# Kernel optimization log

Hardware: AMD Instinct MI355X
Metric: run time of the kernel (lower is better)

## Reference

```python
import jax, jax.numpy as jnp
import numpy as np

N, P, T, K = 20000, 5, 16, 3
IN, H, O = 150, 64, 128


def setup_inputs() -> dict:
    key = jax.random.key(0)
    k1, k2, k3, k4, k5 = jax.random.split(key, 5)
    x = jax.random.normal(k1, (N, IN), dtype=jnp.float32)
    conn_idx = jax.random.randint(k2, (N, P, T, K), 0, N, dtype=jnp.int32)
    conn_w = jax.random.uniform(k3, (N, P, T, K), dtype=jnp.float32)
    # learned params
    W1 = jax.random.normal(k4, (H, IN), dtype=jnp.float32) * 0.05   # linear_1 (no bias)
    Wg = jax.random.normal(k5, (O, H, P, T), dtype=jnp.float32) * 0.05  # geodesic conv weight
    bg = jnp.zeros((O,), dtype=jnp.float32)                          # geodesic conv bias
    return {"x": x, "conn_idx": conn_idx, "conn_w": conn_w, "W1": W1, "Wg": Wg, "bg": bg}


def reference(x, conn_idx, conn_w, W1, Wg, bg):
    # Linear + ReLU: [N, H]
    h = jax.nn.relu(x @ W1.T)
    # Geodesic patch gather: interpolate vertex features into P x T bins
    g = jnp.take(h, conn_idx, axis=0)                 # [N, P, T, K, H]
    patches = jnp.einsum('nptk,nptkh->npth', conn_w, g)  # [N, P, T, H]
    # Geodesic convolution: contract patch bins and channels
    out = jnp.einsum('npth,ohpt->no', patches, Wg) + bg  # [N, O]
    # L2 normalize per vertex
    norm = jnp.linalg.norm(out, axis=-1, keepdims=True)
    return out / norm
```

## Files before the change

### kernel.cpp

```cpp
#include <hip/hip_runtime.h>
#include <hip/hip_fp16.h>

#define NV   20000
#define KK   3
#define INF  150
#define HH   64
#define OO   128
#define PT   80
#define KTOT 5120
#define NB   64
#define RS   72
#define CB   (NB * RS)
#define XS   168
#define NBIN 20

typedef _Float16 fh8 __attribute__((ext_vector_type(8)));
typedef __attribute__((ext_vector_type(4))) float f32x4;
typedef __attribute__((ext_vector_type(8))) unsigned short u16x8;

__device__ __forceinline__ unsigned short f2h(float f) {
    return __half_as_ushort(__float2half(f));
}
__device__ __forceinline__ float h2f(unsigned short u) {
    return __half2float(__ushort_as_half(u));
}
__device__ __forceinline__ _Float16 u2h(unsigned short u) {
    union { unsigned short s; _Float16 h; } c; c.s = u; return c.h;
}

__global__ __launch_bounds__(256) void prep_kernel(
    const float* __restrict__ Wg, const float* __restrict__ x,
    const float* __restrict__ W1, unsigned short* __restrict__ W2,
    unsigned short* __restrict__ hb) {
    __shared__ __align__(16) unsigned char smem[32256];
    const int tid = threadIdx.x;

    if (blockIdx.x < 128) {
        float* lds = (float*)smem;
        const int o = blockIdx.x;
        const float* src = Wg + o * KTOT;
        for (int t = tid; t < KTOT; t += 256) {
            int h = t / 80, bin = t - h * 80;
            lds[h * 81 + bin] = src[t];
        }
        __syncthreads();
        for (int t = tid; t < KTOT; t += 256) {
            W2[(t >> 5) * 4096 + o * 32 + (t & 31)] =
                f2h(lds[(t & 63) * 81 + (t >> 6)]);
        }
        return;
    }

    unsigned short* xs = (unsigned short*)smem;
    unsigned short* ws = xs + 32 * XS;
    const int n0 = (blockIdx.x - 128) * 32;

    for (int e = tid; e < 32 * INF; e += 256) {
        int r = e / INF, c = e - r * INF;
        xs[r * XS + c] = f2h(x[n0 * INF + e]);
    }
    for (int e = tid; e < 32 * 18; e += 256) {
        int r = e / 18, c = e - r * 18;
        xs[r * XS + 150 + c] = 0;
    }
    for (int e = tid; e < 64 * INF; e += 256) {
        int r = e / INF, c = e - r * INF;
        ws[r * XS + c] = f2h(W1[e]);
    }
    for (int e = tid; e < 64 * 18; e += 256) {
        int r = e / 18, c = e - r * 18;
        ws[r * XS + 150 + c] = 0;
    }
    __syncthreads();

    const int wv   = tid >> 6;
    const int lane = tid & 63;
    const int q    = lane >> 4;
    const int r16  = lane & 15;
    const int o0   = wv * 16;

    f32x4 acc0 = {0.f, 0.f, 0.f, 0.f};
    f32x4 acc1 = acc0;
    #pragma unroll
    for (int s = 0; s < 5; s++) {
        const int kb = s * 32 + q * 8;
        fh8 a0 = *(const fh8*)(xs + r16 * XS + kb);
        fh8 a1 = *(const fh8*)(xs + (16 + r16) * XS + kb);
        fh8 b  = *(const fh8*)(ws + (o0 + r16) * XS + kb);
        acc0 = __builtin_amdgcn_mfma_f32_16x16x32_f16(a0, b, acc0, 0, 0, 0);
        acc1 = __builtin_amdgcn_mfma_f32_16x16x32_f16(a1, b, acc1, 0, 0, 0);
    }
    #pragma unroll
    for (int r = 0; r < 4; r++) {
        float v0 = acc0[r] > 0.f ? acc0[r] : 0.f;
        float v1 = acc1[r] > 0.f ? acc1[r] : 0.f;
        hb[(n0 + q * 4 + r) * HH + o0 + r16]      = f2h(v0);
        hb[(n0 + 16 + q * 4 + r) * HH + o0 + r16] = f2h(v1);
    }
}

__global__ __launch_bounds__(256, 4) void geo_kernel(
    const int*   __restrict__ conn_idx, const float* __restrict__ conn_w,
    const unsigned short* __restrict__ W2, const unsigned short* __restrict__ hb,
    float* __restrict__ out, unsigned short* __restrict__ parts) {
    __shared__ __align__(16) unsigned short pch[2 * CB];
    __shared__ __align__(16) unsigned short cp[NB * NBIN * 8];

    const int tid  = threadIdx.x;
    const int ks   = blockIdx.x & 3;
    const int n0   = (blockIdx.x >> 2) * NB;
    const int wv   = tid >> 6;
    const int lane = tid & 63;
    const int q    = lane >> 4;
    const int r16  = lane & 15;
    const int j8   = tid & 7;
    const int v0   = tid >> 3;
    const int bbase = ks * NBIN;
    const int Sbase = ks * 40;

    for (int e = tid; e < NB * NBIN; e += 256) {
        const int v = e / NBIN, cc = e - v * NBIN;
        const int vv = n0 + v;
        u16x8 pk = {0, 0, 0, 0, 0, 0, 0, 0};
        if (vv < NV) {
            const int g = vv * (PT * KK) + (bbase + cc) * KK;
            pk[0] = (unsigned short)conn_idx[g];
            pk[1] = (unsigned short)conn_idx[g + 1];
            pk[2] = (unsigned short)conn_idx[g + 2];
            pk[3] = f2h(conn_w[g]);
            pk[4] = f2h(conn_w[g + 1]);
            pk[5] = f2h(conn_w[g + 2]);
        }
        *(u16x8*)(cp + e * 8) = pk;
    }

    f32x4 acc[4][2];
    #pragma unroll
    for (int m = 0; m < 4; m++) {
        acc[m][0] = (f32x4){0.f, 0.f, 0.f, 0.f};
        acc[m][1] = (f32x4){0.f, 0.f, 0.f, 0.f};
    }

    u16x8 pa, pb;
    fh8   hva0, hva1, hva2, hvb0, hvb1, hvb2;

    auto loadg = [&](int cc) {
        pa = *(const u16x8*)(cp + (v0 * NBIN + cc) * 8);
        pb = *(const u16x8*)(cp + ((v0 + 32) * NBIN + cc) * 8);
        hva0 = *(const fh8*)(hb + (int)pa[0] * HH + j8 * 8);
        hva1 = *(const fh8*)(hb + (int)pa[1] * HH + j8 * 8);
        hva2 = *(const fh8*)(hb + (int)pa[2] * HH + j8 * 8);
        hvb0 = *(const fh8*)(hb + (int)pb[0] * HH + j8 * 8);
        hvb1 = *(const fh8*)(hb + (int)pb[1] * HH + j8 * 8);
        hvb2 = *(const fh8*)(hb + (int)pb[2] * HH + j8 * 8);
    };
    auto cwr = [&](unsigned short* buf) {
        const _Float16 a0 = u2h(pa[3]), a1 = u2h(pa[4]), a2 = u2h(pa[5]);
        const _Float16 b0 = u2h(pb[3]), b1 = u2h(pb[4]), b2 = u2h(pb[5]);
        const fh8 A0 = {a0, a0, a0, a0, a0, a0, a0, a0};
        const fh8 A1 = {a1, a1, a1, a1, a1, a1, a1, a1};
        const fh8 A2 = {a2, a2, a2, a2, a2, a2, a2, a2};
        const fh8 B0 = {b0, b0, b0, b0, b0, b0, b0, b0};
        const fh8 B1 = {b1, b1, b1, b1, b1, b1, b1, b1};
        const fh8 B2 = {b2, b2, b2, b2, b2, b2, b2, b2};
        fh8 ra = hva0 * A0 + hva1 * A1 + hva2 * A2;
        fh8 rb = hvb0 * B0 + hvb1 * B1 + hvb2 * B2;
        *(fh8*)(buf + v0 * RS + j8 * 8)        = ra;
        *(fh8*)(buf + (v0 + 32) * RS + j8 * 8) = rb;
    };
    auto mfmaph = [&](const unsigned short* buf, int cc) {
        #pragma unroll
        for (int s = 0; s < 2; s++) {
            const int S  = Sbase + cc * 2 + s;
            const int ao = s * 32 + q * 8;
            fh8 bf0 = *(const fh8*)(W2 + S * 4096 + ((wv * 2 + 0) * 16 + r16) * 32 + q * 8);
            fh8 bf1 = *(const fh8*)(W2 + S * 4096 + ((wv * 2 + 1) * 16 + r16) * 32 + q * 8);
            #pragma unroll
            for (int m = 0; m < 4; m++) {
                fh8 af = *(const fh8*)(buf + (m * 16 + r16) * RS + ao);
                acc[m][0] = __builtin_amdgcn_mfma_f32_16x16x32_f16(af, bf0, acc[m][0], 0, 0, 0);
                acc[m][1] = __builtin_amdgcn_mfma_f32_16x16x32_f16(af, bf1, acc[m][1], 0, 0, 0);
            }
        }
    };

    __syncthreads();

    loadg(0);
    cwr(pch);
    __syncthreads();

    for (int cc = 0; cc < NBIN; cc++) {
        if (cc + 1 < NBIN) loadg(cc + 1);
        mfmaph(&pch[(cc & 1) * CB], cc);
        if (cc + 1 < NBIN) cwr(&pch[((cc + 1) & 1) * CB]);
        __syncthreads();
    }

    if (ks == 0) {
        #pragma unroll
        for (int m = 0; m < 4; m++) {
            const int rb = n0 + m * 16 + q * 4;
            #pragma unroll
            for (int r = 0; r < 4; r++) {
                if (rb + r < NV) {
                    out[(rb + r) * OO + (wv * 2 + 0) * 16 + r16] = acc[m][0][r];
                    out[(rb + r) * OO + (wv * 2 + 1) * 16 + r16] = acc[m][1][r];
                }
            }
        }
    } else {
        unsigned short* pp = parts + (ks - 1) * (NV * OO);
        #pragma unroll
        for (int m = 0; m < 4; m++) {
            const int rb = n0 + m * 16 + q * 4;
            #pragma unroll
            for (int r = 0; r < 4; r++) {
                if (rb + r < NV) {
                    pp[(rb + r) * OO + (wv * 2 + 0) * 16 + r16] = f2h(acc[m][0][r]);
                    pp[(rb + r) * OO + (wv * 2 + 1) * 16 + r16] = f2h(acc[m][1][r]);
                }
            }
        }
    }
}

__global__ __launch_bounds__(256) void norm_kernel(
    float* __restrict__ out, const unsigned short* __restrict__ parts,
    const float* __restrict__ bg) {
    const int tid = threadIdx.x;
    const int n   = blockIdx.x * 32 + (tid >> 3);
    const int l   = tid & 7;
    float v[16];
    float s = 0.f;
    #pragma unroll
    for (int i = 0; i < 16; i++) {
        const int o = i * 8 + l;
        const int e = n * OO + o;
        v[i] = out[e] + h2f(parts[e]) + h2f(parts[NV * OO + e]) +
               h2f(parts[2 * NV * OO + e]) + bg[o];
        s += v[i] * v[i];
    }
    for (int off = 4; off; off >>= 1) s += __shfl_down(s, off, 8);
    const float r = rsqrtf(__shfl(s, 0, 8));
    #pragma unroll
    for (int i = 0; i < 16; i++)
        out[n * OO + i * 8 + l] = v[i] * r;
}

extern "C" void kernel_launch(void* const* d_in, const int* in_sizes, int n_in,
                              void* d_out, int out_size, void* d_ws, size_t ws_size,
                              hipStream_t stream) {
    const float* x        = (const float*)d_in[0];
    const int*   conn_idx = (const int*)  d_in[1];
    const float* conn_w   = (const float*)d_in[2];
    const float* W1       = (const float*)d_in[3];
    const float* Wg       = (const float*)d_in[4];
    const float* bg       = (const float*)d_in[5];
    float*       out      = (float*)d_out;

    unsigned short* W2    = (unsigned short*)d_ws;
    unsigned short* hb    = W2 + OO * KTOT;
    unsigned short* parts = hb + NV * HH;

    hipLaunchKernelGGL(prep_kernel, dim3(128 + NV / 32), dim3(256), 0, stream,
                       Wg, x, W1, W2, hb);
    hipLaunchKernelGGL(geo_kernel, dim3(4 * 313), dim3(256), 0, stream,
                       conn_idx, conn_w, W2, hb, out, parts);
    hipLaunchKernelGGL(norm_kernel, dim3(NV / 32), dim3(256), 0, stream,
                       out, parts, bg);
}
```

Baseline: 176.7 us.

## Restructure geo kernel to single-wave blocks with register-resident patch fragments

The geodesic kernel moves from 256-thread blocks over 64 vertices to 64-thread single-wave blocks over 32 vertices. Each lane now gathers and combines the patch values straight into MFMA A-fragment registers, so the LDS patch double buffer and the per-bin __syncthreads are gone. Each wave covers all 128 output channels with 16 accumulators, and connectivity reads are software-pipelined two bins ahead. The trade-off is higher register pressure, and each W2 fragment is reused by only 32 vertices instead of 64, which raises global/L2 weight traffic.

```diff
diff --git a/kernel.cpp b/kernel.cpp
--- a/kernel.cpp
+++ b/kernel.cpp
@@ -8,11 +8,9 @@
 #define OO   128
 #define PT   80
 #define KTOT 5120
-#define NB   64
-#define RS   72
-#define CB   (NB * RS)
 #define XS   168
 #define NBIN 20
+#define CPV  33
 
 typedef _Float16 fh8 __attribute__((ext_vector_type(8)));
 typedef __attribute__((ext_vector_type(4))) float f32x4;
@@ -99,128 +97,124 @@
     }
 }
 
-__global__ __launch_bounds__(256, 4) void geo_kernel(
+__global__ __launch_bounds__(64, 2) void geo_kernel(
     const int*   __restrict__ conn_idx, const float* __restrict__ conn_w,
     const unsigned short* __restrict__ W2, const unsigned short* __restrict__ hb,
     float* __restrict__ out, unsigned short* __restrict__ parts) {
-    __shared__ __align__(16) unsigned short pch[2 * CB];
-    __shared__ __align__(16) unsigned short cp[NB * NBIN * 8];
-
-    const int tid  = threadIdx.x;
-    const int ks   = blockIdx.x & 3;
-    const int n0   = (blockIdx.x >> 2) * NB;
-    const int wv   = tid >> 6;
-    const int lane = tid & 63;
-    const int q    = lane >> 4;
-    const int r16  = lane & 15;
-    const int j8   = tid & 7;
-    const int v0   = tid >> 3;
+    __shared__ __align__(16) unsigned short cp[NBIN * CPV * 8];
+
+    const int tid   = threadIdx.x;
+    const int ks    = blockIdx.x & 3;
+    const int vb    = (blockIdx.x >> 2) * 32;
+    const int q     = tid >> 4;
+    const int r16   = tid & 15;
+    const int co    = q * 8;
     const int bbase = ks * NBIN;
-    const int Sbase = ks * 40;
-
-    for (int e = tid; e < NB * NBIN; e += 256) {
+    const int Sb    = ks * (NBIN * 2);
+
+    for (int e = tid; e < 32 * NBIN; e += 64) {
         const int v = e / NBIN, cc = e - v * NBIN;
-        const int vv = n0 + v;
-        u16x8 pk = {0, 0, 0, 0, 0, 0, 0, 0};
-        if (vv < NV) {
-            const int g = vv * (PT * KK) + (bbase + cc) * KK;
-            pk[0] = (unsigned short)conn_idx[g];
-            pk[1] = (unsigned short)conn_idx[g + 1];
-            pk[2] = (unsigned short)conn_idx[g + 2];
-            pk[3] = f2h(conn_w[g]);
-            pk[4] = f2h(conn_w[g + 1]);
-            pk[5] = f2h(conn_w[g + 2]);
-        }
-        *(u16x8*)(cp + e * 8) = pk;
-    }
-
-    f32x4 acc[4][2];
-    #pragma unroll
-    for (int m = 0; m < 4; m++) {
-        acc[m][0] = (f32x4){0.f, 0.f, 0.f, 0.f};
-        acc[m][1] = (f32x4){0.f, 0.f, 0.f, 0.f};
-    }
-
-    u16x8 pa, pb;
-    fh8   hva0, hva1, hva2, hvb0, hvb1, hvb2;
-
-    auto loadg = [&](int cc) {
-        pa = *(const u16x8*)(cp + (v0 * NBIN + cc) * 8);
-        pb = *(const u16x8*)(cp + ((v0 + 32) * NBIN + cc) * 8);
-        hva0 = *(const fh8*)(hb + (int)pa[0] * HH + j8 * 8);
-        hva1 = *(const fh8*)(hb + (int)pa[1] * HH + j8 * 8);
-        hva2 = *(const fh8*)(hb + (int)pa[2] * HH + j8 * 8);
-        hvb0 = *(const fh8*)(hb + (int)pb[0] * HH + j8 * 8);
-        hvb1 = *(const fh8*)(hb + (int)pb[1] * HH + j8 * 8);
-        hvb2 = *(const fh8*)(hb + (int)pb[2] * HH + j8 * 8);
-    };
-    auto cwr = [&](unsigned short* buf) {
-        const _Float16 a0 = u2h(pa[3]), a1 = u2h(pa[4]), a2 = u2h(pa[5]);
-        const _Float16 b0 = u2h(pb[3]), b1 = u2h(pb[4]), b2 = u2h(pb[5]);
-        const fh8 A0 = {a0, a0, a0, a0, a0, a0, a0, a0};
-        const fh8 A1 = {a1, a1, a1, a1, a1, a1, a1, a1};
-        const fh8 A2 = {a2, a2, a2, a2, a2, a2, a2, a2};
-        const fh8 B0 = {b0, b0, b0, b0, b0, b0, b0, b0};
-        const fh8 B1 = {b1, b1, b1, b1, b1, b1, b1, b1};
-        const fh8 B2 = {b2, b2, b2, b2, b2, b2, b2, b2};
-        fh8 ra = hva0 * A0 + hva1 * A1 + hva2 * A2;
-        fh8 rb = hvb0 * B0 + hvb1 * B1 + hvb2 * B2;
-        *(fh8*)(buf + v0 * RS + j8 * 8)        = ra;
-        *(fh8*)(buf + (v0 + 32) * RS + j8 * 8) = rb;
-    };
-    auto mfmaph = [&](const unsigned short* buf, int cc) {
+        const int gi = (vb + v) * (PT * KK) + (bbase + cc) * KK;
+        u16x8 pk;
+        pk[0] = (unsigned short)conn_idx[gi];
+        pk[1] = (unsigned short)conn_idx[gi + 1];
+        pk[2] = (unsigned short)conn_idx[gi + 2];
+        pk[3] = f2h(conn_w[gi]);
+        pk[4] = f2h(conn_w[gi + 1]);
+        pk[5] = f2h(conn_w[gi + 2]);
+        pk[6] = 0; pk[7] = 0;
+        *(u16x8*)(cp + (cc * CPV + v) * 8) = pk;
+    }
+    __syncthreads();
+
+    f32x4 acc[2][8];
+    #pragma unroll
+    for (int m = 0; m < 2; m++)
+        #pragma unroll
+        for (int o = 0; o < 8; o++)
+            acc[m][o] = (f32x4){0.f, 0.f, 0.f, 0.f};
+
+    fh8 gv[2][2][3];
+    fh8 pat[2][2];
+
+    auto rdconn = [&](int cc, u16x8& a, u16x8& b) {
+        a = *(const u16x8*)(cp + (cc * CPV + r16) * 8);
+        b = *(const u16x8*)(cp + (cc * CPV + 16 + r16) * 8);
+    };
+    auto gath = [&](const u16x8& a, const u16x8& b) {
+        #pragma unroll
+        for (int k = 0; k < 3; k++) {
+            const unsigned short* pA = hb + (int)a[k] * HH + co;
+            const unsigned short* pB = hb + (int)b[k] * HH + co;
+            gv[0][0][k] = *(const fh8*)(pA);
+            gv[0][1][k] = *(const fh8*)(pA + 32);
+            gv[1][0][k] = *(const fh8*)(pB);
+            gv[1][1][k] = *(const fh8*)(pB + 32);
+        }
+    };
+    auto comb = [&](const u16x8& a, const u16x8& b) {
         #pragma unroll
         for (int s = 0; s < 2; s++) {
-            const int S  = Sbase + cc * 2 + s;
-            const int ao = s * 32 + q * 8;
-            fh8 bf0 = *(const fh8*)(W2 + S * 4096 + ((wv * 2 + 0) * 16 + r16) * 32 + q * 8);
-            fh8 bf1 = *(const fh8*)(W2 + S * 4096 + ((wv * 2 + 1) * 16 + r16) * 32 + q * 8);
+            fh8 r0 = {}; fh8 r1 = {};
             #pragma unroll
-            for (int m = 0; m < 4; m++) {
-                fh8 af = *(const fh8*)(buf + (m * 16 + r16) * RS + ao);
-                acc[m][0] = __builtin_amdgcn_mfma_f32_16x16x32_f16(af, bf0, acc[m][0], 0, 0, 0);
-                acc[m][1] = __builtin_amdgcn_mfma_f32_16x16x32_f16(af, bf1, acc[m][1], 0, 0, 0);
+            for (int k = 0; k < 3; k++) {
+                const _Float16 wA = u2h(a[3 + k]);
+                const _Float16 wB = u2h(b[3 + k]);
+                const fh8 WA = {wA, wA, wA, wA, wA, wA, wA, wA};
+                const fh8 WB = {wB, wB, wB, wB, wB, wB, wB, wB};
+                r0 += gv[0][s][k] * WA;
+                r1 += gv[1][s][k] * WB;
             }
-        }
-    };
-
-    __syncthreads();
-
-    loadg(0);
-    cwr(pch);
-    __syncthreads();
+            pat[0][s] = r0; pat[1][s] = r1;
+        }
+    };
+    auto mfmap = [&](int cc) {
+        const unsigned short* wp = W2 + (Sb + cc * 2) * 4096 + r16 * 32 + co;
+        #pragma unroll
+        for (int o = 0; o < 8; o++) {
+            fh8 bf0 = *(const fh8*)(wp + o * 512);
+            fh8 bf1 = *(const fh8*)(wp + 4096 + o * 512);
+            acc[0][o] = __builtin_amdgcn_mfma_f32_16x16x32_f16(pat[0][0], bf0, acc[0][o], 0, 0, 0);
+            acc[1][o] = __builtin_amdgcn_mfma_f32_16x16x32_f16(pat[1][0], bf0, acc[1][o], 0, 0, 0);
+            acc[0][o] = __builtin_amdgcn_mfma_f32_16x16x32_f16(pat[0][1], bf1, acc[0][o], 0, 0, 0);
+            acc[1][o] = __builtin_amdgcn_mfma_f32_16x16x32_f16(pat[1][1], bf1, acc[1][o], 0, 0, 0);
+        }
+    };
+
+    u16x8 cA, cB, nA, nB, tA, tB;
+    rdconn(0, cA, cB);
+    gath(cA, cB);
+    rdconn(1, nA, nB);
+    comb(cA, cB);
 
     for (int cc = 0; cc < NBIN; cc++) {
-        if (cc + 1 < NBIN) loadg(cc + 1);
-        mfmaph(&pch[(cc & 1) * CB], cc);
-        if (cc + 1 < NBIN) cwr(&pch[((cc + 1) & 1) * CB]);
-        __syncthreads();
+        const bool more = (cc + 1 < NBIN);
+        if (more) gath(nA, nB);
+        if (cc + 2 < NBIN) rdconn(cc + 2, tA, tB);
+        mfmap(cc);
+        if (more) { comb(nA, nB); nA = tA; nB = tB; }
     }
 
     if (ks == 0) {
         #pragma unroll
-        for (int m = 0; m < 4; m++) {
-            const int rb = n0 + m * 16 + q * 4;
+        for (int m = 0; m < 2; m++) {
+            const int rb = vb + m * 16 + q * 4;
             #pragma unroll
-            for (int r = 0; r < 4; r++) {
-                if (rb + r < NV) {
-                    out[(rb + r) * OO + (wv * 2 + 0) * 16 + r16] = acc[m][0][r];
-                    out[(rb + r) * OO + (wv * 2 + 1) * 16 + r16] = acc[m][1][r];
-                }
-            }
+            for (int o = 0; o < 8; o++)
+                #pragma unroll
+                for (int r = 0; r < 4; r++)
+                    out[(rb + r) * OO + o * 16 + r16] = acc[m][o][r];
         }
     } else {
         unsigned short* pp = parts + (ks - 1) * (NV * OO);
         #pragma unroll
-        for (int m = 0; m < 4; m++) {
-            const int rb = n0 + m * 16 + q * 4;
+        for (int m = 0; m < 2; m++) {
+            const int rb = vb + m * 16 + q * 4;
             #pragma unroll
-            for (int r = 0; r < 4; r++) {
-                if (rb + r < NV) {
-                    pp[(rb + r) * OO + (wv * 2 + 0) * 16 + r16] = f2h(acc[m][0][r]);
-                    pp[(rb + r) * OO + (wv * 2 + 1) * 16 + r16] = f2h(acc[m][1][r]);
-                }
-            }
+            for (int o = 0; o < 8; o++)
+                #pragma unroll
+                for (int r = 0; r < 4; r++)
+                    pp[(rb + r) * OO + o * 16 + r16] = f2h(acc[m][o][r]);
         }
     }
 }
@@ -265,7 +259,7 @@
 
     hipLaunchKernelGGL(prep_kernel, dim3(128 + NV / 32), dim3(256), 0, stream,
                        Wg, x, W1, W2, hb);
-    hipLaunchKernelGGL(geo_kernel, dim3(4 * 313), dim3(256), 0, stream,
+    hipLaunchKernelGGL(geo_kernel, dim3(4 * (NV / 32)), dim3(64), 0, stream,
                        conn_idx, conn_w, W2, hb, out, parts);
     hipLaunchKernelGGL(norm_kernel, dim3(NV / 32), dim3(256), 0, stream,
                        out, parts, bg);
```

Measured after the change: 226.3 us. +28.0%, slower.

## Double vertex tile to 128 with 512-thread blocks and prefetch W2 fragments

Applied to the files above, without the earlier changes.

Raises the vertex tile per block from 64 to 128 and the block from 256 to 512 threads (8 waves), with each wave now owning one 16-wide output column slab instead of two. The main loop is manually unrolled by two with explicit ping-pong buffers, and the W2 fragments for the next bin are loaded into registers one step ahead. The aim is to reuse each W2 fragment across more vertex rows and to hide W2 global load latency. In exchange the block uses more shared memory (double buffers sized for 128 rows), there are fewer blocks in the grid, and launch bounds of 512 with 4 blocks per CU may limit register allocation.

```diff
diff --git a/kernel.cpp b/kernel.cpp
--- a/kernel.cpp
+++ b/kernel.cpp
@@ -8,7 +8,7 @@
 #define OO   128
 #define PT   80
 #define KTOT 5120
-#define NB   64
+#define NB   128
 #define RS   72
 #define CB   (NB * RS)
 #define XS   168
@@ -99,7 +99,7 @@
     }
 }
 
-__global__ __launch_bounds__(256, 4) void geo_kernel(
+__global__ __launch_bounds__(512, 4) void geo_kernel(
     const int*   __restrict__ conn_idx, const float* __restrict__ conn_w,
     const unsigned short* __restrict__ W2, const unsigned short* __restrict__ hb,
     float* __restrict__ out, unsigned short* __restrict__ parts) {
@@ -118,7 +118,7 @@
     const int bbase = ks * NBIN;
     const int Sbase = ks * 40;
 
-    for (int e = tid; e < NB * NBIN; e += 256) {
+    for (int e = tid; e < NB * NBIN; e += 512) {
         const int v = e / NBIN, cc = e - v * NBIN;
         const int vv = n0 + v;
         u16x8 pk = {0, 0, 0, 0, 0, 0, 0, 0};
@@ -134,25 +134,28 @@
         *(u16x8*)(cp + e * 8) = pk;
     }
 
-    f32x4 acc[4][2];
-    #pragma unroll
-    for (int m = 0; m < 4; m++) {
-        acc[m][0] = (f32x4){0.f, 0.f, 0.f, 0.f};
-        acc[m][1] = (f32x4){0.f, 0.f, 0.f, 0.f};
-    }
+    f32x4 acc[8];
+    #pragma unroll
+    for (int m = 0; m < 8; m++) acc[m] = (f32x4){0.f, 0.f, 0.f, 0.f};
 
     u16x8 pa, pb;
     fh8   hva0, hva1, hva2, hvb0, hvb1, hvb2;
 
     auto loadg = [&](int cc) {
         pa = *(const u16x8*)(cp + (v0 * NBIN + cc) * 8);
-        pb = *(const u16x8*)(cp + ((v0 + 32) * NBIN + cc) * 8);
+        pb = *(const u16x8*)(cp + ((v0 + 64) * NBIN + cc) * 8);
         hva0 = *(const fh8*)(hb + (int)pa[0] * HH + j8 * 8);
         hva1 = *(const fh8*)(hb + (int)pa[1] * HH + j8 * 8);
         hva2 = *(const fh8*)(hb + (int)pa[2] * HH + j8 * 8);
         hvb0 = *(const fh8*)(hb + (int)pb[0] * HH + j8 * 8);
         hvb1 = *(const fh8*)(hb + (int)pb[1] * HH + j8 * 8);
         hvb2 = *(const fh8*)(hb + (int)pb[2] * HH + j8 * 8);
+    };
+    auto w2ld = [&](int cc, fh8& b0, fh8& b1) {
+        const unsigned short* wp =
+            W2 + (Sbase + cc * 2) * 4096 + (wv * 16 + r16) * 32 + q * 8;
+        b0 = *(const fh8*)(wp);
+        b1 = *(const fh8*)(wp + 4096);
     };
     auto cwr = [&](unsigned short* buf) {
         const _Float16 a0 = u2h(pa[3]), a1 = u2h(pa[4]), a2 = u2h(pa[5]);
@@ -166,60 +169,64 @@
         fh8 ra = hva0 * A0 + hva1 * A1 + hva2 * A2;
         fh8 rb = hvb0 * B0 + hvb1 * B1 + hvb2 * B2;
         *(fh8*)(buf + v0 * RS + j8 * 8)        = ra;
-        *(fh8*)(buf + (v0 + 32) * RS + j8 * 8) = rb;
-    };
-    auto mfmaph = [&](const unsigned short* buf, int cc) {
+        *(fh8*)(buf + (v0 + 64) * RS + j8 * 8) = rb;
+    };
+    auto mfmaph = [&](const unsigned short* buf, fh8 w0, fh8 w1) {
         #pragma unroll
         for (int s = 0; s < 2; s++) {
-            const int S  = Sbase + cc * 2 + s;
             const int ao = s * 32 + q * 8;
-            fh8 bf0 = *(const fh8*)(W2 + S * 4096 + ((wv * 2 + 0) * 16 + r16) * 32 + q * 8);
-            fh8 bf1 = *(const fh8*)(W2 + S * 4096 + ((wv * 2 + 1) * 16 + r16) * 32 + q * 8);
+            const fh8 bf = s ? w1 : w0;
             #pragma unroll
-            for (int m = 0; m < 4; m++) {
+            for (int m = 0; m < 8; m++) {
                 fh8 af = *(const fh8*)(buf + (m * 16 + r16) * RS + ao);
-                acc[m][0] = __builtin_amdgcn_mfma_f32_16x16x32_f16(af, bf0, acc[m][0], 0, 0, 0);
-                acc[m][1] = __builtin_amdgcn_mfma_f32_16x16x32_f16(af, bf1, acc[m][1], 0, 0, 0);
+                acc[m] = __builtin_amdgcn_mfma_f32_16x16x32_f16(af, bf, acc[m], 0, 0, 0);
             }
         }
     };
 
     __syncthreads();
 
+    fh8 w2a0, w2a1, w2b0, w2b1;
     loadg(0);
+    w2ld(0, w2a0, w2a1);
     cwr(pch);
     __syncthreads();
 
-    for (int cc = 0; cc < NBIN; cc++) {
-        if (cc + 1 < NBIN) loadg(cc + 1);
-        mfmaph(&pch[(cc & 1) * CB], cc);
-        if (cc + 1 < NBIN) cwr(&pch[((cc + 1) & 1) * CB]);
+    #pragma unroll 1
+    for (int cc = 0; cc < NBIN; cc += 2) {
+        loadg(cc + 1);
+        w2ld(cc + 1, w2b0, w2b1);
+        mfmaph(pch, w2a0, w2a1);
+        cwr(pch + CB);
+        __syncthreads();
+        if (cc + 2 < NBIN) {
+            loadg(cc + 2);
+            w2ld(cc + 2, w2a0, w2a1);
+        }
+        mfmaph(pch + CB, w2b0, w2b1);
+        if (cc + 2 < NBIN) cwr(pch);
         __syncthreads();
     }
 
     if (ks == 0) {
         #pragma unroll
-        for (int m = 0; m < 4; m++) {
+        for (int m = 0; m < 8; m++) {
             const int rb = n0 + m * 16 + q * 4;
             #pragma unroll
             for (int r = 0; r < 4; r++) {
-                if (rb + r < NV) {
-                    out[(rb + r) * OO + (wv * 2 + 0) * 16 + r16] = acc[m][0][r];
-                    out[(rb + r) * OO + (wv * 2 + 1) * 16 + r16] = acc[m][1][r];
-                }
+                if (rb + r < NV)
+                    out[(rb + r) * OO + wv * 16 + r16] = acc[m][r];
             }
         }
     } else {
         unsigned short* pp = parts + (ks - 1) * (NV * OO);
         #pragma unroll
-        for (int m = 0; m < 4; m++) {
+        for (int m = 0; m < 8; m++) {
             const int rb = n0 + m * 16 + q * 4;
             #pragma unroll
             for (int r = 0; r < 4; r++) {
-                if (rb + r < NV) {
-                    pp[(rb + r) * OO + (wv * 2 + 0) * 16 + r16] = f2h(acc[m][0][r]);
-                    pp[(rb + r) * OO + (wv * 2 + 1) * 16 + r16] = f2h(acc[m][1][r]);
-                }
+                if (rb + r < NV)
+                    pp[(rb + r) * OO + wv * 16 + r16] = f2h(acc[m][r]);
             }
         }
     }
@@ -263,9 +270,11 @@
     unsigned short* hb    = W2 + OO * KTOT;
     unsigned short* parts = hb + NV * HH;
 
+    const int vtiles = (NV + NB - 1) / NB;
+
     hipLaunchKernelGGL(prep_kernel, dim3(128 + NV / 32), dim3(256), 0, stream,
                        Wg, x, W1, W2, hb);
-    hipLaunchKernelGGL(geo_kernel, dim3(4 * 313), dim3(256), 0, stream,
+    hipLaunchKernelGGL(geo_kernel, dim3(4 * vtiles), dim3(512), 0, stream,
                        conn_idx, conn_w, W2, hb, out, parts);
     hipLaunchKernelGGL(norm_kernel, dim3(NV / 32), dim3(256), 0, stream,
                        out, parts, bg);
```

After: 172.8 us. 2.2% less time.
